# Kernel tuning notes

Hardware: AMD Instinct MI355X
Metric: run time of the kernel (lower is better)

The kernel has to match this reference:

```python
import jax, jax.numpy as jnp
import numpy as np

SUB = 40   # subframe_size
NSUB = 4   # nb_subframes


def _glu(x, w):
    return x * jax.nn.sigmoid(x @ w.T)


def _gru(x, h, w_ih, w_hh):
    # torch.nn.GRUCell (bias=False): gates ordered r, z, n
    H = h.shape[-1]
    gi = x @ w_ih.T
    gh = h @ w_hh.T
    r = jax.nn.sigmoid(gi[:, :H] + gh[:, :H])
    z = jax.nn.sigmoid(gi[:, H:2 * H] + gh[:, H:2 * H])
    n = jnp.tanh(gi[:, 2 * H:] + r * gh[:, 2 * H:])
    return (1.0 - z) * n + z * h


def _fargan_forward(features, period, p):
    B, T, _ = features.shape
    period = jnp.clip(period, 32, 254)

    # ---- FARGANCond ----
    f = features[:, 2:, :]                               # [B, T-2, 20]
    pidx = jnp.clip(period[:, 2:] - 32, 0, 223)
    pe = p['pembed'][pidx]                               # [B, T-2, 12]
    x = jnp.tanh(jnp.concatenate([f, pe], -1) @ p['fd1_w'].T)   # [B, T-2, 64]
    y = jax.lax.conv_general_dilated(
        x.transpose(0, 2, 1), p['fconv1_w'], (1,), 'VALID',
        dimension_numbers=('NCH', 'OIH', 'NCH'))
    y = jnp.tanh(y).transpose(0, 2, 1)                   # [B, T-4, 128]
    cond = jnp.tanh(y @ p['fd2_w'].T)                    # [B, T-4, 320]

    nb_frames = T - 4
    cond_steps = cond.reshape(B, nb_frames, NSUB, 80)
    cond_steps = cond_steps.transpose(1, 2, 0, 3).reshape(nb_frames * NSUB, B, 80)
    pitch = period[:, 3:3 + nb_frames]                   # conv-center aligned pitch
    pitch_steps = jnp.repeat(pitch.T, NSUB, axis=0)      # [steps, B]

    rng = jnp.arange(SUB + 4)

    def step(carry, inp):
        exc_mem, prev_pred, s1, s2, s3, fwc_state = carry
        cond80, per = inp
        gain = 0.2 + 0.8 * jax.nn.sigmoid(cond80 @ p['cg_w'].T + p['cg_b'])
        gain = jnp.clip(gain, 0.001, 20.0)               # [B, 1]
        idx = 256 - per[:, None] + rng[None, :] - 2
        idx = idx - (idx >= 256) * per[:, None]
        idx = jnp.clip(idx, 0, 255)
        pred = jnp.take_along_axis(exc_mem, idx, axis=1) / (1e-5 + gain)  # [B, 44]
        prev = exc_mem[:, -SUB:] / (1e-5 + gain)         # [B, 40]
        tmp = jnp.concatenate([cond80, pred, prev], 1)   # [B, 164]
        fpitch = pred[:, 2:-2]                           # [B, 40]
        xcat = jnp.concatenate([fwc_state, tmp], 1)      # [B, 328]
        fwc_out = _glu(jnp.tanh(xcat @ p['fwc_w'].T), p['fwc_glu_w'])  # [B, 192]
        new_fwc_state = xcat[:, 164:]
        pg = jax.nn.sigmoid(fwc_out @ p['gout_w'].T + p['gout_b'])     # [B, 4]
        s1n = _gru(jnp.concatenate([fwc_out, pg[:, 0:1] * fpitch, prev], 1), s1, p['g1_ih'], p['g1_hh'])
        g1 = _glu(s1n, p['glu1_w'])
        s2n = _gru(jnp.concatenate([g1, pg[:, 1:2] * fpitch, prev], 1), s2, p['g2_ih'], p['g2_hh'])
        g2 = _glu(s2n, p['glu2_w'])
        s3n = _gru(jnp.concatenate([g2, pg[:, 2:3] * fpitch, prev], 1), s3, p['g3_ih'], p['g3_hh'])
        g3 = _glu(s3n, p['glu3_w'])
        skip_in = jnp.concatenate([g1, g2, g3, fwc_out, pg[:, 3:4] * fpitch, prev], 1)  # [B, 688+80]
        skip = _glu(jnp.tanh(skip_in @ p['skip_w'].T), p['skip_glu_w'])
        sig = jnp.tanh(skip @ p['sig_w'].T) * gain       # [B, 40]
        exc_mem = jnp.concatenate([exc_mem[:, SUB:], sig], 1)
        prev_pred = jnp.concatenate([prev_pred[:, SUB:], fpitch], 1)
        return (exc_mem, prev_pred, s1n, s2n, s3n, new_fwc_state), sig

    dt = features.dtype
    carry0 = (jnp.zeros((B, 256), dt), jnp.zeros((B, 256), dt),
              jnp.zeros((B, 160), dt), jnp.zeros((B, 128), dt),
              jnp.zeros((B, 128), dt), jnp.zeros((B, 164), dt))
    _, sigs = jax.lax.scan(jax.checkpoint(step), carry0, (cond_steps, pitch_steps))
    return sigs.transpose(1, 0, 2).reshape(B, -1)        # [B, nb_frames*160]


def _w(key, out_dim, in_dim):
    return jax.random.normal(key, (out_dim, in_dim), jnp.float32) / np.sqrt(in_dim)


def setup_inputs() -> dict:
    key = jax.random.key(0)
    ks = jax.random.split(key, 24)
    B, T = 128, 504
    d = {}
    d['features'] = jax.random.normal(ks[0], (B, T, 20), jnp.float32)
    d['period'] = jax.random.randint(ks[1], (B, T), 32, 255)
    d['pembed'] = jax.random.normal(ks[2], (224, 12), jnp.float32) * 0.3
    d['fd1_w'] = _w(ks[3], 64, 32)
    d['fconv1_w'] = jax.random.normal(ks[4], (128, 64, 3), jnp.float32) / np.sqrt(192.0)
    d['fd2_w'] = _w(ks[5], 320, 128)
    d['cg_w'] = _w(ks[6], 1, 80)
    d['cg_b'] = jnp.zeros((1,), jnp.float32)
    d['fwc_w'] = _w(ks[7], 192, 328)
    d['fwc_glu_w'] = _w(ks[8], 192, 192)
    d['g1_ih'] = _w(ks[9], 480, 272)
    d['g1_hh'] = _w(ks[10], 480, 160)
    d['glu1_w'] = _w(ks[11], 160, 160)
    d['g2_ih'] = _w(ks[12], 384, 240)
    d['g2_hh'] = _w(ks[13], 384, 128)
    d['glu2_w'] = _w(ks[14], 128, 128)
    d['g3_ih'] = _w(ks[15], 384, 208)
    d['g3_hh'] = _w(ks[16], 384, 128)
    d['glu3_w'] = _w(ks[17], 128, 128)
    d['skip_w'] = _w(ks[18], 128, 688)
    d['skip_glu_w'] = _w(ks[19], 128, 128)
    d['sig_w'] = _w(ks[20], 40, 128)
    d['gout_w'] = _w(ks[21], 4, 192)
    d['gout_b'] = jnp.zeros((4,), jnp.float32)
    return d


def reference(features, period, pembed, fd1_w, fconv1_w, fd2_w, cg_w, cg_b,
              fwc_w, fwc_glu_w, g1_ih, g1_hh, glu1_w, g2_ih, g2_hh, glu2_w,
              g3_ih, g3_hh, glu3_w, skip_w, skip_glu_w, sig_w, gout_w, gout_b):
    p = dict(pembed=pembed, fd1_w=fd1_w, fconv1_w=fconv1_w, fd2_w=fd2_w,
             cg_w=cg_w, cg_b=cg_b, fwc_w=fwc_w, fwc_glu_w=fwc_glu_w,
             g1_ih=g1_ih, g1_hh=g1_hh, glu1_w=glu1_w,
             g2_ih=g2_ih, g2_hh=g2_hh, glu2_w=glu2_w,
             g3_ih=g3_ih, g3_hh=g3_hh, glu3_w=glu3_w,
             skip_w=skip_w, skip_glu_w=skip_glu_w, sig_w=sig_w,
             gout_w=gout_w, gout_b=gout_b)
    return _fargan_forward(features, period, p)
```

## Files before the change

### kernel.cpp

```cpp
#include <hip/hip_runtime.h>
#include <hip/hip_fp16.h>
#include <math.h>


#define DEV __device__ __forceinline__

DEV float sigm(float x) { return 1.0f / (1.0f + __expf(-x)); }
DEV float tanh_f(float x) { return 1.0f - 2.0f / (__expf(2.0f * x) + 1.0f); }

typedef _Float16 h2v __attribute__((ext_vector_type(2)));

#if defined(__has_builtin)
#if __has_builtin(__builtin_amdgcn_fdot2)
#define HAVE_FDOT2 1
#endif
#endif

DEV float fdot2(h2v a, h2v b, float c) {
#ifdef HAVE_FDOT2
    return __builtin_amdgcn_fdot2(a, b, c, false);
#else
    return c + (float)a[0] * (float)b[0] + (float)a[1] * (float)b[1];
#endif
}

constexpr size_t STEPS = 2000;
constexpr size_t OFF_X     = 0;
constexpr size_t OFF_Y     = 4200000;
constexpr size_t OFF_GAIN  = 12392000;
constexpr size_t OFF_CONDH = 12648000;
constexpr size_t OFF_W     = 22888000;

constexpr size_t W_FWC     = 0;
constexpr size_t W_FWCGLU  = W_FWC    + 192*352;
constexpr size_t W_GOUT    = W_FWCGLU + 192*192;
constexpr size_t W_G1IH    = W_GOUT   + 4*192;
constexpr size_t W_G1HH    = W_G1IH   + 480*272;
constexpr size_t W_GLU1    = W_G1HH   + 480*160;
constexpr size_t W_G2IH    = W_GLU1   + 160*160;
constexpr size_t W_G2HH    = W_G2IH   + 384*240;
constexpr size_t W_GLU2    = W_G2HH   + 384*128;
constexpr size_t W_G3IH    = W_GLU2   + 128*128;
constexpr size_t W_G3HH    = W_G3IH   + 384*208;
constexpr size_t W_GLU3    = W_G3HH   + 384*128;
constexpr size_t W_SKIP    = W_GLU3   + 128*128;
constexpr size_t W_SKIPGLU = W_SKIP   + 128*704;
constexpr size_t W_SIG     = W_SKIPGLU+ 128*128;

constexpr int WL_FWCGLU = 0;
constexpr int WL_GLU2   = 4608;
constexpr int WL_GLU3   = 6656;
constexpr int WL_TOT    = 8704;

__global__ void k_pack_h(const float* __restrict__ src, __half* __restrict__ dst,
                         int OUT, int K, int KP8) {
    int t = blockIdx.x * 256 + threadIdx.x;
    if (t >= OUT * KP8) return;
    int j = t % OUT;
    int k8 = t / OUT;
    __half* d = dst + (size_t)t * 8;
#pragma unroll
    for (int i = 0; i < 8; ++i) {
        int k = k8 * 8 + i;
        d[i] = (k < K) ? __float2half(src[(size_t)j * K + k]) : __float2half(0.0f);
    }
}

__global__ void k_feat(const float* __restrict__ features, const int* __restrict__ period,
                       const float* __restrict__ pembed, const float* __restrict__ fd1,
                       float* __restrict__ xbuf) {
    int t = blockIdx.x * 256 + threadIdx.x;
    const int total = 128 * 502 * 64;
    if (t >= total) return;
    int o = t & 63;
    int r = t >> 6;
    int ft = r % 502;
    int b = r / 502;
    const float* f = features + ((size_t)b * 504 + ft + 2) * 20;
    int per = period[b * 504 + ft + 2];
    per = min(max(per, 32), 254);
    const float* pe = pembed + (per - 32) * 12;
    const float* w = fd1 + o * 32;
    float acc = 0.0f;
#pragma unroll
    for (int i = 0; i < 20; ++i) acc += f[i] * w[i];
#pragma unroll
    for (int i = 0; i < 12; ++i) acc += pe[i] * w[20 + i];
    xbuf[t] = tanh_f(acc);
}

__global__ void k_conv(const float* __restrict__ xbuf, const float* __restrict__ fconv1,
                       float* __restrict__ ybuf) {
    int t = blockIdx.x * 256 + threadIdx.x;
    const int total = 128 * 500 * 128;
    if (t >= total) return;
    int oc = t & 127;
    int r = t >> 7;
    int tt = r % 500;
    int b = r / 500;
    const float* xp = xbuf + ((size_t)b * 502 + tt) * 64;
    const float* w = fconv1 + oc * 192;
    float acc = 0.0f;
#pragma unroll 8
    for (int i = 0; i < 64; ++i) {
        acc += xp[i] * w[i * 3 + 0];
        acc += xp[64 + i] * w[i * 3 + 1];
        acc += xp[128 + i] * w[i * 3 + 2];
    }
    ybuf[t] = tanh_f(acc);
}

__global__ void k_cond(const float* __restrict__ ybuf, const float* __restrict__ fd2,
                       __half* __restrict__ cond) {
    int b = blockIdx.x / 50;
    int t0 = (blockIdx.x % 50) * 10;
    int tid = threadIdx.x;
    __shared__ float yl[1280];
    for (int i = tid; i < 1280; i += 320)
        yl[i] = ybuf[((size_t)b * 500 + t0) * 128 + i];
    __syncthreads();
    const float* w = fd2 + tid * 128;
    float acc[10];
#pragma unroll
    for (int q = 0; q < 10; ++q) acc[q] = 0.0f;
#pragma unroll 4
    for (int k = 0; k < 128; ++k) {
        float wv = w[k];
#pragma unroll
        for (int q = 0; q < 10; ++q) acc[q] += wv * yl[q * 128 + k];
    }
#pragma unroll
    for (int q = 0; q < 10; ++q)
        cond[((size_t)b * 500 + t0 + q) * 320 + tid] = __float2half(tanh_f(acc[q]));
}

__global__ void k_gain(const __half* __restrict__ cond, const float* __restrict__ cgw,
                       const float* __restrict__ cgb, float* __restrict__ gains) {
    int t = blockIdx.x * 256 + threadIdx.x;
    const int total = 128 * 2000;
    if (t >= total) return;
    int s = t % 2000;
    int b = t / 2000;
    int frame = s >> 2, sub = s & 3;
    const __half* c = cond + ((size_t)b * 500 + frame) * 320 + sub * 80;
    float acc = 0.0f;
#pragma unroll 8
    for (int i = 0; i < 80; ++i) acc += __half2float(c[i]) * cgw[i];
    float g = 0.2f + 0.8f * sigm(acc + cgb[0]);
    g = fminf(20.0f, fmaxf(0.001f, g));
    gains[t] = g;
}

DEV void dot8h(uint4 w, uint4 x, float& a0, float& a1) {
    const h2v* wv = (const h2v*)&w;
    const h2v* xv = (const h2v*)&x;
    a0 = fdot2(wv[0], xv[0], a0);
    a1 = fdot2(wv[1], xv[1], a1);
    a0 = fdot2(wv[2], xv[2], a0);
    a1 = fdot2(wv[3], xv[3], a1);
}

template <int OUT, int KP8, int S>
DEV void mv_partial(const uint4* __restrict__ WT, const __half* __restrict__ x,
                    float* __restrict__ part, int tid) {
    static_assert(KP8 % S == 0, "KP8 % S");
    static_assert(OUT * S <= 1024, "threads");
    constexpr int KS8 = KP8 / S;
    if (tid < OUT * S) {
        int j = tid % OUT;
        int sl = tid / OUT;
        const uint4* w = WT + (size_t)sl * KS8 * OUT + j;
        const uint4* xx = (const uint4*)x + (size_t)sl * KS8;
        float a0 = 0.0f, a1 = 0.0f;
#pragma unroll 4
        for (int k = 0; k < KS8; ++k) dot8h(w[(size_t)k * OUT], xx[k], a0, a1);
        part[tid] = a0 + a1;
    }
}

template <int OUT, int KP8, int S>
DEV void mv_partial_l(const uint4* wl, const __half* __restrict__ x,
                      float* __restrict__ part, int tid) {
    constexpr int KS8 = KP8 / S;
    if (tid < OUT * S) {
        int j = tid % OUT;
        int sl = tid / OUT;
        const uint4* w = wl + (size_t)sl * KS8 * OUT + j;
        const uint4* xx = (const uint4*)x + (size_t)sl * KS8;
        float a0 = 0.0f, a1 = 0.0f;
#pragma unroll
        for (int k = 0; k < KS8; ++k) dot8h(w[(size_t)k * OUT], xx[k], a0, a1);
        part[tid] = a0 + a1;
    }
}

template <int OUT, int KP8A, int KP8B>
DEV void gru_partial(const uint4* __restrict__ wa, const __half* __restrict__ xa,
                     const uint4* __restrict__ wb, const __half* __restrict__ xb,
                     float* __restrict__ pa, float* __restrict__ pb, int tid) {
    static_assert((KP8A % 2 == 0) && (KP8B % 2 == 0), "even");
    constexpr int KA = KP8A / 2, KB = KP8B / 2;
    if (tid < OUT * 2) {
        int j = tid % OUT;
        int sl = tid / OUT;
        {
            const uint4* w = wa + (size_t)sl * KA * OUT + j;
            const uint4* xx = (const uint4*)xa + (size_t)sl * KA;
            float a0 = 0.0f, a1 = 0.0f;
#pragma unroll 4
            for (int k = 0; k < KA; ++k) dot8h(w[(size_t)k * OUT], xx[k], a0, a1);
            pa[tid] = a0 + a1;
        }
        {
            const uint4* w = wb + (size_t)sl * KB * OUT + j;
            const uint4* xx = (const uint4*)xb + (size_t)sl * KB;
            float b0 = 0.0f, b1 = 0.0f;
#pragma unroll 4
            for (int k = 0; k < KB; ++k) dot8h(w[(size_t)k * OUT], xx[k], b0, b1);
            pb[tid] = b0 + b1;
        }
    }
}

template <int H>
DEV void gru_update(const float* __restrict__ pa, const float* __restrict__ pb,
                    float* __restrict__ s, __half* __restrict__ sh, int tid) {
    constexpr int OUT = 3 * H;
    if (tid < H) {
        float gi_r = pa[tid] + pa[OUT + tid];
        float gh_r = pb[tid] + pb[OUT + tid];
        float gi_z = pa[H + tid] + pa[OUT + H + tid];
        float gh_z = pb[H + tid] + pb[OUT + H + tid];
        float gi_n = pa[2 * H + tid] + pa[OUT + 2 * H + tid];
        float gh_n = pb[2 * H + tid] + pb[OUT + 2 * H + tid];
        float r = sigm(gi_r + gh_r);
        float z = sigm(gi_z + gh_z);
        float n = tanh_f(gi_n + r * gh_n);
        float v = (1.0f - z) * n + z * s[tid];
        s[tid] = v;
        sh[tid] = __float2half(v);
    }
}

__global__ __launch_bounds__(1024) void fargan_main(const float* __restrict__ ws,
                                                    const int* __restrict__ period,
                                                    const float* __restrict__ goutb,
                                                    float* __restrict__ out) {
    const int b = blockIdx.x;
    const int tid = threadIdx.x;

    const __half* cond = (const __half*)(ws + OFF_CONDH);
    const float* gains = ws + OFF_GAIN;
    const __half* whb  = (const __half*)(ws + OFF_W);
    const uint4* wFWC     = (const uint4*)(whb + W_FWC);
    const uint4* wFWCGLU  = (const uint4*)(whb + W_FWCGLU);
    const uint4* wGOUT    = (const uint4*)(whb + W_GOUT);
    const uint4* wG1IH    = (const uint4*)(whb + W_G1IH);
    const uint4* wG1HH    = (const uint4*)(whb + W_G1HH);
    const uint4* wGLU1    = (const uint4*)(whb + W_GLU1);
    const uint4* wG2IH    = (const uint4*)(whb + W_G2IH);
    const uint4* wG2HH    = (const uint4*)(whb + W_G2HH);
    const uint4* wGLU2    = (const uint4*)(whb + W_GLU2);
    const uint4* wG3IH    = (const uint4*)(whb + W_G3IH);
    const uint4* wG3HH    = (const uint4*)(whb + W_G3HH);
    const uint4* wGLU3    = (const uint4*)(whb + W_GLU3);
    const uint4* wSKIP    = (const uint4*)(whb + W_SKIP);
    const uint4* wSKIPGLU = (const uint4*)(whb + W_SKIPGLU);
    const uint4* wSIG     = (const uint4*)(whb + W_SIG);

    __shared__ __align__(16) uint4 wlds[WL_TOT];

    __shared__ __align__(16) __half xcat_h[352];
    __shared__ __align__(16) __half inb_h[272];
    __shared__ __align__(16) __half fwcpre_h[192], fwcout_h[192];
    __shared__ __align__(16) __half s1_h[160], s2_h[128], s3_h[128];
    __shared__ __align__(16) __half g1_h[160], g2_h[128], g3_h[128];
    __shared__ __align__(16) __half skipin_h[704], skippre_h[128], skipout_h[128];
    __shared__ __align__(16) float exc[256];
    __shared__ __align__(16) float s1[160], s2[128], s3[128];
    __shared__ __align__(16) float partA[1024], partB[1024];
    __shared__ __align__(16) float fwcpre[192];
    __shared__ __align__(16) float pg[4];
    __shared__ __align__(16) float skippre[128];
    __shared__ __align__(16) float sigraw[40];

    for (int i = tid; i < 4608; i += 1024) wlds[WL_FWCGLU + i] = wFWCGLU[i];
    for (int i = tid; i < 2048; i += 1024) wlds[WL_GLU2 + i] = wGLU2[i];
    for (int i = tid; i < 2048; i += 1024) wlds[WL_GLU3 + i] = wGLU3[i];

    const int j2 = tid % 384;
    const int sl2 = (tid < 768) ? (tid / 384) : 0;
    const uint4* g2b = wG2HH + (size_t)sl2 * 8 * 384 + j2;
    const uint4 c0 = g2b[0 * 384];
    const uint4 c1 = g2b[1 * 384];
    const uint4 c2 = g2b[2 * 384];
    const uint4 c3 = g2b[3 * 384];
    const uint4 c4 = g2b[4 * 384];
    const uint4 c5 = g2b[5 * 384];
    const uint4 c6 = g2b[6 * 384];
    const uint4 c7 = g2b[7 * 384];

    for (int i = tid; i < 256; i += 1024) exc[i] = 0.0f;
    if (tid < 160) { s1[tid] = 0.0f; s1_h[tid] = __float2half(0.0f); }
    if (tid < 128) { s2[tid] = 0.0f; s3[tid] = 0.0f;
                     s2_h[tid] = __float2half(0.0f); s3_h[tid] = __float2half(0.0f); }
    if (tid < 164) xcat_h[tid] = __float2half(0.0f);
    if (tid >= 328 && tid < 352) xcat_h[tid] = __float2half(0.0f);
    if (tid >= 688 && tid < 704) skipin_h[tid] = __float2half(0.0f);
    __syncthreads();

    for (int s = 0; s < (int)STEPS; ++s) {
        const int frame = s >> 2;
        const float gain = gains[(size_t)b * 2000 + s];
        const float ig = 1.0f / (1e-5f + gain);
        int per = period[b * 504 + 3 + frame];
        per = min(max(per, 32), 254);

        if (tid < 80) {
            xcat_h[164 + tid] = cond[((size_t)b * 500 + frame) * 320 + (s & 3) * 80 + tid];
        } else if (tid >= 128 && tid < 172) {
            int j = tid - 128;
            int idx = 254 - per + j;
            if (idx >= 256) idx -= per;
            idx = min(255, max(0, idx));
            xcat_h[244 + j] = __float2half(exc[idx] * ig);
        } else if (tid >= 192 && tid < 232) {
            xcat_h[288 + tid - 192] = __float2half(exc[216 + tid - 192] * ig);
        }
        __syncthreads();

        mv_partial<192, 44, 4>(wFWC, xcat_h, partA, tid);
        __syncthreads();
        if (tid < 192) {
            float a = partA[tid] + partA[192 + tid] + partA[384 + tid] + partA[576 + tid];
            float t = tanh_f(a);
            fwcpre[tid] = t;
            fwcpre_h[tid] = __float2half(t);
        }
        __syncthreads();

        mv_partial_l<192, 24, 4>(wlds + WL_FWCGLU, fwcpre_h, partA, tid);
        if (tid >= 768 && tid < 800) {
            int t2 = tid - 768;
            int j = t2 & 3, sl = t2 >> 2;
            const uint4* w = wGOUT + (sl * 3) * 4 + j;
            const uint4* xx = (const uint4*)fwcpre_h + sl * 3;
            float a0 = 0.0f, a1 = 0.0f;
#pragma unroll
            for (int k = 0; k < 3; ++k) dot8h(w[k * 4], xx[k], a0, a1);
            partB[t2] = a0 + a1;
        } else if (tid >= 832 && tid < 996) {
            xcat_h[tid - 832] = xcat_h[tid - 832 + 164];
        }
        __syncthreads();

        if (tid < 192) {
            float a = partA[tid] + partA[192 + tid] + partA[384 + tid] + partA[576 + tid];
            float v = fwcpre[tid] * sigm(a);
            __half vh = __float2half(v);
            fwcout_h[tid] = vh;
            inb_h[tid] = vh;
        } else if (tid < 232) {
            float a = goutb[0];
#pragma unroll
            for (int sl = 0; sl < 8; ++sl) a += partB[sl * 4];
            inb_h[tid] = __float2half(sigm(a) * __half2float(xcat_h[246 + tid - 192]));
        } else if (tid < 272) {
            inb_h[tid] = xcat_h[288 + tid - 232];
        } else if (tid >= 960 && tid < 964) {
            int j = tid - 960;
            float a = goutb[j];
#pragma unroll
            for (int sl = 0; sl < 8; ++sl) a += partB[sl * 4 + j];
            pg[j] = sigm(a);
        }
        __syncthreads();

        gru_partial<480, 34, 20>(wG1IH, inb_h, wG1HH, s1_h, partA, partB, tid);
        __syncthreads();
        gru_update<160>(partA, partB, s1, s1_h, tid);
        __syncthreads();

        mv_partial<160, 20, 4>(wGLU1, s1_h, partA, tid);
        __syncthreads();
        if (tid < 160) {
            float a = partA[tid] + partA[160 + tid] + partA[320 + tid] + partA[480 + tid];
            float v = s1[tid] * sigm(a);
            __half vh = __float2half(v);
            g1_h[tid] = vh;
            inb_h[tid] = vh;
        } else if (tid < 200) {
            inb_h[tid] = __float2half(pg[1] * __half2float(xcat_h[246 + tid - 160]));
        } else if (tid < 240) {
            inb_h[tid] = xcat_h[288 + tid - 200];
        }
        __syncthreads();

        if (tid < 768) {
            constexpr int KA = 15;
            {
                const uint4* w = wG2IH + (size_t)sl2 * KA * 384 + j2;
                const uint4* xx = (const uint4*)inb_h + (size_t)sl2 * KA;
                float a0 = 0.0f, a1 = 0.0f;
#pragma unroll 4
                for (int k = 0; k < KA; ++k) dot8h(w[(size_t)k * 384], xx[k], a0, a1);
                partA[tid] = a0 + a1;
            }
            {
                const uint4* xb = (const uint4*)s2_h + (size_t)sl2 * 8;
                float b0 = 0.0f, b1 = 0.0f;
                dot8h(c0, xb[0], b0, b1);
                dot8h(c1, xb[1], b0, b1);
                dot8h(c2, xb[2], b0, b1);
                dot8h(c3, xb[3], b0, b1);
                dot8h(c4, xb[4], b0, b1);
                dot8h(c5, xb[5], b0, b1);
                dot8h(c6, xb[6], b0, b1);
                dot8h(c7, xb[7], b0, b1);
                partB[tid] = b0 + b1;
            }
        }
        __syncthreads();
        gru_update<128>(partA, partB, s2, s2_h, tid);
        __syncthreads();

        mv_partial_l<128, 16, 8>(wlds + WL_GLU2, s2_h, partA, tid);
        __syncthreads();
        if (tid < 128) {
            float a = 0.0f;
#pragma unroll
            for (int sl = 0; sl < 8; ++sl) a += partA[sl * 128 + tid];
            float v = s2[tid] * sigm(a);
            __half vh = __float2half(v);
            g2_h[tid] = vh;
            inb_h[tid] = vh;
        } else if (tid < 168) {
            inb_h[tid] = __float2half(pg[2] * __half2float(xcat_h[246 + tid - 128]));
        } else if (tid < 208) {
            inb_h[tid] = xcat_h[288 + tid - 168];
        }
        __syncthreads();

        gru_partial<384, 26, 16>(wG3IH, inb_h, wG3HH, s3_h, partA, partB, tid);
        __syncthreads();
        gru_update<128>(partA, partB, s3, s3_h, tid);
        __syncthreads();

        mv_partial_l<128, 16, 8>(wlds + WL_GLU3, s3_h, partA, tid);
        __syncthreads();
        if (tid < 128) {
            float a = 0.0f;
#pragma unroll
            for (int sl = 0; sl < 8; ++sl) a += partA[sl * 128 + tid];
            float v = s3[tid] * sigm(a);
            __half vh = __float2half(v);
            g3_h[tid] = vh;
            skipin_h[288 + tid] = vh;
        } else if (tid < 288) {
            skipin_h[tid - 128] = g1_h[tid - 128];
        } else if (tid < 416) {
            skipin_h[160 + tid - 288] = g2_h[tid - 288];
        } else if (tid < 608) {
            skipin_h[tid] = fwcout_h[tid - 416];
        } else if (tid < 648) {
            skipin_h[tid] = __float2half(pg[3] * __half2float(xcat_h[246 + tid - 608]));
        } else if (tid < 688) {
            skipin_h[tid] = xcat_h[288 + tid - 648];
        }
        __syncthreads();

        mv_partial<128, 88, 8>(wSKIP, skipin_h, partA, tid);
        __syncthreads();
        if (tid < 128) {
            float a = 0.0f;
#pragma unroll
            for (int sl = 0; sl < 8; ++sl) a += partA[sl * 128 + tid];
            float t = tanh_f(a);
            skippre[tid] = t;
            skippre_h[tid] = __float2half(t);
        }
        __syncthreads();

        mv_partial<128, 16, 8>(wSKIPGLU, skippre_h, partA, tid);
        __syncthreads();
        if (tid < 128) {
            float a = 0.0f;
#pragma unroll
            for (int sl = 0; sl < 8; ++sl) a += partA[sl * 128 + tid];
            skipout_h[tid] = __float2half(skippre[tid] * sigm(a));
        }
        __syncthreads();

        mv_partial<40, 16, 8>(wSIG, skipout_h, partA, tid);
        __syncthreads();
        float keep = (tid < 216) ? exc[tid + 40] : 0.0f;
        if (tid < 40) {
            float a = 0.0f;
#pragma unroll
            for (int sl = 0; sl < 8; ++sl) a += partA[sl * 40 + tid];
            sigraw[tid] = tanh_f(a) * gain;
        }
        __syncthreads();
        if (tid < 216) {
            exc[tid] = keep;
        } else if (tid < 256) {
            float sv = sigraw[tid - 216];
            exc[tid] = sv;
            out[(size_t)b * 80000 + (size_t)s * 40 + (tid - 216)] = sv;
        }
        __syncthreads();
    }
}

extern "C" void kernel_launch(void* const* d_in, const int* in_sizes, int n_in,
                              void* d_out, int out_size, void* d_ws, size_t ws_size,
                              hipStream_t stream) {
    const float* features = (const float*)d_in[0];
    const int*   period   = (const int*)d_in[1];
    const float* pembed   = (const float*)d_in[2];
    const float* fd1_w    = (const float*)d_in[3];
    const float* fconv1_w = (const float*)d_in[4];
    const float* fd2_w    = (const float*)d_in[5];
    const float* cg_w     = (const float*)d_in[6];
    const float* cg_b     = (const float*)d_in[7];
    const float* fwc_w    = (const float*)d_in[8];
    const float* fwc_glu  = (const float*)d_in[9];
    const float* g1_ih    = (const float*)d_in[10];
    const float* g1_hh    = (const float*)d_in[11];
    const float* glu1_w   = (const float*)d_in[12];
    const float* g2_ih    = (const float*)d_in[13];
    const float* g2_hh    = (const float*)d_in[14];
    const float* glu2_w   = (const float*)d_in[15];
    const float* g3_ih    = (const float*)d_in[16];
    const float* g3_hh    = (const float*)d_in[17];
    const float* glu3_w   = (const float*)d_in[18];
    const float* skip_w   = (const float*)d_in[19];
    const float* skip_glu = (const float*)d_in[20];
    const float* sig_w    = (const float*)d_in[21];
    const float* gout_w   = (const float*)d_in[22];
    const float* gout_b   = (const float*)d_in[23];

    float* ws = (float*)d_ws;
    float* out = (float*)d_out;
    __half* wh = (__half*)(ws + OFF_W);

    struct PW { const float* src; size_t off; int out, k, kpad; };
    const PW pws[15] = {
        {fwc_w,    W_FWC,     192, 328, 352}, {fwc_glu, W_FWCGLU, 192, 192, 192},
        {gout_w,   W_GOUT,      4, 192, 192}, {g1_ih,   W_G1IH,   480, 272, 272},
        {g1_hh,    W_G1HH,    480, 160, 160}, {glu1_w,  W_GLU1,   160, 160, 160},
        {g2_ih,    W_G2IH,    384, 240, 240}, {g2_hh,   W_G2HH,   384, 128, 128},
        {glu2_w,   W_GLU2,    128, 128, 128}, {g3_ih,   W_G3IH,   384, 208, 208},
        {g3_hh,    W_G3HH,    384, 128, 128}, {glu3_w,  W_GLU3,   128, 128, 128},
        {skip_w,   W_SKIP,    128, 688, 704}, {skip_glu,W_SKIPGLU,128, 128, 128},
        {sig_w,    W_SIG,      40, 128, 128},
    };
    for (int i = 0; i < 15; ++i) {
        int kp8 = pws[i].kpad / 8;
        int n = pws[i].out * kp8;
        k_pack_h<<<(n + 255) / 256, 256, 0, stream>>>(pws[i].src, wh + pws[i].off,
                                                      pws[i].out, pws[i].k, kp8);
    }

    {
        int n = 128 * 502 * 64;
        k_feat<<<(n + 255) / 256, 256, 0, stream>>>(features, period, pembed, fd1_w,
                                                    ws + OFF_X);
    }
    {
        int n = 128 * 500 * 128;
        k_conv<<<(n + 255) / 256, 256, 0, stream>>>(ws + OFF_X, fconv1_w, ws + OFF_Y);
    }
    k_cond<<<128 * 50, 320, 0, stream>>>(ws + OFF_Y, fd2_w, (__half*)(ws + OFF_CONDH));
    {
        int n = 128 * 2000;
        k_gain<<<(n + 255) / 256, 256, 0, stream>>>((const __half*)(ws + OFF_CONDH),
                                                    cg_w, cg_b, ws + OFF_GAIN);
    }

    fargan_main<<<128, 1024, 0, stream>>>(ws, period, gout_b, out);
}
```

Before: 34.19 ms.

## Interleave K-split weight layout and reduce partial sums with wave shuffles

Weights are repacked so the K-slices of one output row sit in adjacent lanes. Each matvec then reduces its partial sums with __shfl_xor instead of writing them to shared memory and summing in a separate phase. This removes many __syncthreads barriers and shared-memory round trips per subframe step in the sequential recurrent loop. It also fuses the post-processing (tanh, sigmoid gating, the gain output) into the matvec phase and changes some split factors, for example GLU2 and GLU3 go from 8 slices to 4, which may lower parallelism per matvec.

```diff
diff --git a/kernel.cpp b/kernel.cpp
--- a/kernel.cpp
+++ b/kernel.cpp
@@ -53,15 +53,19 @@
 constexpr int WL_TOT    = 8704;
 
 __global__ void k_pack_h(const float* __restrict__ src, __half* __restrict__ dst,
-                         int OUT, int K, int KP8) {
+                         int OUT, int K, int KP8, int S) {
     int t = blockIdx.x * 256 + threadIdx.x;
     if (t >= OUT * KP8) return;
     int j = t % OUT;
-    int k8 = t / OUT;
-    __half* d = dst + (size_t)t * 8;
+    int c = t / OUT;
+    int KS8 = KP8 / S;
+    int sl = c / KS8;
+    int kk = c % KS8;
+    size_t di = (size_t)kk * (OUT * S) + (size_t)j * S + sl;
+    __half* d = dst + di * 8;
 #pragma unroll
     for (int i = 0; i < 8; ++i) {
-        int k = k8 * 8 + i;
+        int k = c * 8 + i;
         d[i] = (k < K) ? __float2half(src[(size_t)j * K + k]) : __float2half(0.0f);
     }
 }
@@ -161,81 +165,74 @@
 }
 
 template <int OUT, int KP8, int S>
-DEV void mv_partial(const uint4* __restrict__ WT, const __half* __restrict__ x,
-                    float* __restrict__ part, int tid) {
-    static_assert(KP8 % S == 0, "KP8 % S");
-    static_assert(OUT * S <= 1024, "threads");
+DEV float mv_w(const uint4* __restrict__ WT, const __half* __restrict__ x, int tid) {
+    static_assert(64 % S == 0, "S divides wave");
     constexpr int KS8 = KP8 / S;
-    if (tid < OUT * S) {
-        int j = tid % OUT;
-        int sl = tid / OUT;
-        const uint4* w = WT + (size_t)sl * KS8 * OUT + j;
-        const uint4* xx = (const uint4*)x + (size_t)sl * KS8;
+    constexpr int TH = OUT * S;
+    const uint4* w = WT + tid;
+    const uint4* xx = (const uint4*)x + (tid % S) * KS8;
+    float a0 = 0.0f, a1 = 0.0f;
+#pragma unroll 4
+    for (int k = 0; k < KS8; ++k) dot8h(w[(size_t)k * TH], xx[k], a0, a1);
+    float p = a0 + a1;
+    if (S >= 2) p += __shfl_xor(p, 1);
+    if (S >= 4) p += __shfl_xor(p, 2);
+    if (S >= 8) p += __shfl_xor(p, 4);
+    return p;
+}
+
+template <int OUT, int KP8, int S>
+DEV float mv_w_l(const uint4* wl, const __half* __restrict__ x, int tid) {
+    constexpr int KS8 = KP8 / S;
+    constexpr int TH = OUT * S;
+    const uint4* w = wl + tid;
+    const uint4* xx = (const uint4*)x + (tid % S) * KS8;
+    float a0 = 0.0f, a1 = 0.0f;
+#pragma unroll
+    for (int k = 0; k < KS8; ++k) dot8h(w[(size_t)k * TH], xx[k], a0, a1);
+    float p = a0 + a1;
+    if (S >= 2) p += __shfl_xor(p, 1);
+    if (S >= 4) p += __shfl_xor(p, 2);
+    if (S >= 8) p += __shfl_xor(p, 4);
+    return p;
+}
+
+template <int OUT, int KP8A, int KP8B>
+DEV void gru_w(const uint4* __restrict__ wa, const __half* __restrict__ xa,
+               const uint4* __restrict__ wb, const __half* __restrict__ xb,
+               float* __restrict__ gi, float* __restrict__ gh, int tid) {
+    constexpr int KA = KP8A / 2, KB = KP8B / 2;
+    constexpr int TH = OUT * 2;
+    const int sl = tid & 1, j = tid >> 1;
+    float pA, pB;
+    {
+        const uint4* w = wa + tid;
+        const uint4* xx = (const uint4*)xa + sl * KA;
         float a0 = 0.0f, a1 = 0.0f;
 #pragma unroll 4
-        for (int k = 0; k < KS8; ++k) dot8h(w[(size_t)k * OUT], xx[k], a0, a1);
-        part[tid] = a0 + a1;
-    }
-}
-
-template <int OUT, int KP8, int S>
-DEV void mv_partial_l(const uint4* wl, const __half* __restrict__ x,
-                      float* __restrict__ part, int tid) {
-    constexpr int KS8 = KP8 / S;
-    if (tid < OUT * S) {
-        int j = tid % OUT;
-        int sl = tid / OUT;
-        const uint4* w = wl + (size_t)sl * KS8 * OUT + j;
-        const uint4* xx = (const uint4*)x + (size_t)sl * KS8;
-        float a0 = 0.0f, a1 = 0.0f;
-#pragma unroll
-        for (int k = 0; k < KS8; ++k) dot8h(w[(size_t)k * OUT], xx[k], a0, a1);
-        part[tid] = a0 + a1;
-    }
-}
-
-template <int OUT, int KP8A, int KP8B>
-DEV void gru_partial(const uint4* __restrict__ wa, const __half* __restrict__ xa,
-                     const uint4* __restrict__ wb, const __half* __restrict__ xb,
-                     float* __restrict__ pa, float* __restrict__ pb, int tid) {
-    static_assert((KP8A % 2 == 0) && (KP8B % 2 == 0), "even");
-    constexpr int KA = KP8A / 2, KB = KP8B / 2;
-    if (tid < OUT * 2) {
-        int j = tid % OUT;
-        int sl = tid / OUT;
-        {
-            const uint4* w = wa + (size_t)sl * KA * OUT + j;
-            const uint4* xx = (const uint4*)xa + (size_t)sl * KA;
-            float a0 = 0.0f, a1 = 0.0f;
+        for (int k = 0; k < KA; ++k) dot8h(w[(size_t)k * TH], xx[k], a0, a1);
+        pA = a0 + a1;
+        pA += __shfl_xor(pA, 1);
+    }
+    {
+        const uint4* w = wb + tid;
+        const uint4* xx = (const uint4*)xb + sl * KB;
+        float b0 = 0.0f, b1 = 0.0f;
 #pragma unroll 4
-            for (int k = 0; k < KA; ++k) dot8h(w[(size_t)k * OUT], xx[k], a0, a1);
-            pa[tid] = a0 + a1;
-        }
-        {
-            const uint4* w = wb + (size_t)sl * KB * OUT + j;
-            const uint4* xx = (const uint4*)xb + (size_t)sl * KB;
-            float b0 = 0.0f, b1 = 0.0f;
-#pragma unroll 4
-            for (int k = 0; k < KB; ++k) dot8h(w[(size_t)k * OUT], xx[k], b0, b1);
-            pb[tid] = b0 + b1;
-        }
-    }
+        for (int k = 0; k < KB; ++k) dot8h(w[(size_t)k * TH], xx[k], b0, b1);
+        pB = b0 + b1;
+        pB += __shfl_xor(pB, 1);
+    }
+    if (sl == 0) { gi[j] = pA; gh[j] = pB; }
 }
 
 template <int H>
-DEV void gru_update(const float* __restrict__ pa, const float* __restrict__ pb,
-                    float* __restrict__ s, __half* __restrict__ sh, int tid) {
-    constexpr int OUT = 3 * H;
+DEV void gru_upd(const float* __restrict__ gi, const float* __restrict__ gh,
+                 float* __restrict__ s, __half* __restrict__ sh, int tid) {
     if (tid < H) {
-        float gi_r = pa[tid] + pa[OUT + tid];
-        float gh_r = pb[tid] + pb[OUT + tid];
-        float gi_z = pa[H + tid] + pa[OUT + H + tid];
-        float gh_z = pb[H + tid] + pb[OUT + H + tid];
-        float gi_n = pa[2 * H + tid] + pa[OUT + 2 * H + tid];
-        float gh_n = pb[2 * H + tid] + pb[OUT + 2 * H + tid];
-        float r = sigm(gi_r + gh_r);
-        float z = sigm(gi_z + gh_z);
-        float n = tanh_f(gi_n + r * gh_n);
+        float r = sigm(gi[tid] + gh[tid]);
+        float z = sigm(gi[H + tid] + gh[H + tid]);
+        float n = tanh_f(gi[2 * H + tid] + r * gh[2 * H + tid]);
         float v = (1.0f - z) * n + z * s[tid];
         s[tid] = v;
         sh[tid] = __float2half(v);
@@ -278,27 +275,25 @@
     __shared__ __align__(16) __half skipin_h[704], skippre_h[128], skipout_h[128];
     __shared__ __align__(16) float exc[256];
     __shared__ __align__(16) float s1[160], s2[128], s3[128];
-    __shared__ __align__(16) float partA[1024], partB[1024];
+    __shared__ __align__(16) float gi_f[480], gh_f[480];
     __shared__ __align__(16) float fwcpre[192];
     __shared__ __align__(16) float pg[4];
     __shared__ __align__(16) float skippre[128];
-    __shared__ __align__(16) float sigraw[40];
 
     for (int i = tid; i < 4608; i += 1024) wlds[WL_FWCGLU + i] = wFWCGLU[i];
     for (int i = tid; i < 2048; i += 1024) wlds[WL_GLU2 + i] = wGLU2[i];
     for (int i = tid; i < 2048; i += 1024) wlds[WL_GLU3 + i] = wGLU3[i];
 
-    const int j2 = tid % 384;
-    const int sl2 = (tid < 768) ? (tid / 384) : 0;
-    const uint4* g2b = wG2HH + (size_t)sl2 * 8 * 384 + j2;
-    const uint4 c0 = g2b[0 * 384];
-    const uint4 c1 = g2b[1 * 384];
-    const uint4 c2 = g2b[2 * 384];
-    const uint4 c3 = g2b[3 * 384];
-    const uint4 c4 = g2b[4 * 384];
-    const uint4 c5 = g2b[5 * 384];
-    const uint4 c6 = g2b[6 * 384];
-    const uint4 c7 = g2b[7 * 384];
+    const int tcl = (tid < 768) ? tid : 0;
+    const uint4* g2b = wG2HH + tcl;
+    const uint4 c0 = g2b[0 * 768];
+    const uint4 c1 = g2b[1 * 768];
+    const uint4 c2 = g2b[2 * 768];
+    const uint4 c3 = g2b[3 * 768];
+    const uint4 c4 = g2b[4 * 768];
+    const uint4 c5 = g2b[5 * 768];
+    const uint4 c6 = g2b[6 * 768];
+    const uint4 c7 = g2b[7 * 768];
 
     for (int i = tid; i < 256; i += 1024) exc[i] = 0.0f;
     if (tid < 160) { s1[tid] = 0.0f; s1_h[tid] = __float2half(0.0f); }
@@ -316,6 +311,7 @@
         int per = period[b * 504 + 3 + frame];
         per = min(max(per, 32), 254);
 
+        float keep = (tid < 216) ? exc[tid + 40] : 0.0f;
         if (tid < 80) {
             xcat_h[164 + tid] = cond[((size_t)b * 500 + frame) * 320 + (s & 3) * 80 + tid];
         } else if (tid >= 128 && tid < 172) {
@@ -329,185 +325,180 @@
         }
         __syncthreads();
 
-        mv_partial<192, 44, 4>(wFWC, xcat_h, partA, tid);
-        __syncthreads();
-        if (tid < 192) {
-            float a = partA[tid] + partA[192 + tid] + partA[384 + tid] + partA[576 + tid];
-            float t = tanh_f(a);
-            fwcpre[tid] = t;
-            fwcpre_h[tid] = __float2half(t);
-        }
-        __syncthreads();
-
-        mv_partial_l<192, 24, 4>(wlds + WL_FWCGLU, fwcpre_h, partA, tid);
-        if (tid >= 768 && tid < 800) {
+        if (tid < 768) {
+            float p = mv_w<192, 44, 4>(wFWC, xcat_h, tid);
+            if ((tid & 3) == 0) {
+                int j = tid >> 2;
+                float t = tanh_f(p);
+                fwcpre[j] = t;
+                fwcpre_h[j] = __float2half(t);
+            }
+        }
+        __syncthreads();
+
+        if (tid < 768) {
+            float p = mv_w_l<192, 24, 4>(wlds + WL_FWCGLU, fwcpre_h, tid);
+            if ((tid & 3) == 0) {
+                int j = tid >> 2;
+                float v = fwcpre[j] * sigm(p);
+                __half vh = __float2half(v);
+                fwcout_h[j] = vh;
+                inb_h[j] = vh;
+            }
+        } else if (tid < 800) {
             int t2 = tid - 768;
-            int j = t2 & 3, sl = t2 >> 2;
-            const uint4* w = wGOUT + (sl * 3) * 4 + j;
-            const uint4* xx = (const uint4*)fwcpre_h + sl * 3;
+            const uint4* w = wGOUT + t2;
+            const uint4* xx = (const uint4*)fwcpre_h + (t2 & 7) * 3;
             float a0 = 0.0f, a1 = 0.0f;
-#pragma unroll
-            for (int k = 0; k < 3; ++k) dot8h(w[k * 4], xx[k], a0, a1);
-            partB[t2] = a0 + a1;
+            dot8h(w[0 * 32], xx[0], a0, a1);
+            dot8h(w[1 * 32], xx[1], a0, a1);
+            dot8h(w[2 * 32], xx[2], a0, a1);
+            float p = a0 + a1;
+            p += __shfl_xor(p, 1);
+            p += __shfl_xor(p, 2);
+            p += __shfl_xor(p, 4);
+            if ((t2 & 7) == 0) pg[t2 >> 3] = sigm(p + goutb[t2 >> 3]);
         } else if (tid >= 832 && tid < 996) {
             xcat_h[tid - 832] = xcat_h[tid - 832 + 164];
         }
         __syncthreads();
 
-        if (tid < 192) {
-            float a = partA[tid] + partA[192 + tid] + partA[384 + tid] + partA[576 + tid];
-            float v = fwcpre[tid] * sigm(a);
-            __half vh = __float2half(v);
-            fwcout_h[tid] = vh;
-            inb_h[tid] = vh;
-        } else if (tid < 232) {
-            float a = goutb[0];
-#pragma unroll
-            for (int sl = 0; sl < 8; ++sl) a += partB[sl * 4];
-            inb_h[tid] = __float2half(sigm(a) * __half2float(xcat_h[246 + tid - 192]));
-        } else if (tid < 272) {
-            inb_h[tid] = xcat_h[288 + tid - 232];
-        } else if (tid >= 960 && tid < 964) {
-            int j = tid - 960;
-            float a = goutb[j];
-#pragma unroll
-            for (int sl = 0; sl < 8; ++sl) a += partB[sl * 4 + j];
-            pg[j] = sigm(a);
-        }
-        __syncthreads();
-
-        gru_partial<480, 34, 20>(wG1IH, inb_h, wG1HH, s1_h, partA, partB, tid);
-        __syncthreads();
-        gru_update<160>(partA, partB, s1, s1_h, tid);
-        __syncthreads();
-
-        mv_partial<160, 20, 4>(wGLU1, s1_h, partA, tid);
-        __syncthreads();
-        if (tid < 160) {
-            float a = partA[tid] + partA[160 + tid] + partA[320 + tid] + partA[480 + tid];
-            float v = s1[tid] * sigm(a);
-            __half vh = __float2half(v);
-            g1_h[tid] = vh;
-            inb_h[tid] = vh;
-        } else if (tid < 200) {
-            inb_h[tid] = __float2half(pg[1] * __half2float(xcat_h[246 + tid - 160]));
-        } else if (tid < 240) {
-            inb_h[tid] = xcat_h[288 + tid - 200];
+        if (tid < 80) {
+            inb_h[192 + tid] = (tid < 40)
+                ? __float2half(pg[0] * __half2float(xcat_h[246 + tid]))
+                : xcat_h[288 + tid - 40];
+        }
+        __syncthreads();
+
+        if (tid < 960)
+            gru_w<480, 34, 20>(wG1IH, inb_h, wG1HH, s1_h, gi_f, gh_f, tid);
+        __syncthreads();
+        gru_upd<160>(gi_f, gh_f, s1, s1_h, tid);
+        __syncthreads();
+
+        if (tid < 640) {
+            float p = mv_w<160, 20, 4>(wGLU1, s1_h, tid);
+            if ((tid & 3) == 0) {
+                int j = tid >> 2;
+                float v = s1[j] * sigm(p);
+                __half vh = __float2half(v);
+                g1_h[j] = vh;
+                inb_h[j] = vh;
+            }
+        } else if (tid < 720) {
+            int t = tid - 640;
+            inb_h[160 + t] = (t < 40)
+                ? __float2half(pg[1] * __half2float(xcat_h[246 + t]))
+                : xcat_h[288 + t - 40];
         }
         __syncthreads();
 
         if (tid < 768) {
-            constexpr int KA = 15;
+            const int sl = tid & 1, j = tid >> 1;
+            float pA, pB;
             {
-                const uint4* w = wG2IH + (size_t)sl2 * KA * 384 + j2;
-                const uint4* xx = (const uint4*)inb_h + (size_t)sl2 * KA;
+                const uint4* w = wG2IH + tid;
+                const uint4* xx = (const uint4*)inb_h + sl * 15;
                 float a0 = 0.0f, a1 = 0.0f;
 #pragma unroll 4
-                for (int k = 0; k < KA; ++k) dot8h(w[(size_t)k * 384], xx[k], a0, a1);
-                partA[tid] = a0 + a1;
+                for (int k = 0; k < 15; ++k) dot8h(w[(size_t)k * 768], xx[k], a0, a1);
+                pA = a0 + a1;
+                pA += __shfl_xor(pA, 1);
             }
             {
-                const uint4* xb = (const uint4*)s2_h + (size_t)sl2 * 8;
+                const uint4* xx = (const uint4*)s2_h + sl * 8;
                 float b0 = 0.0f, b1 = 0.0f;
-                dot8h(c0, xb[0], b0, b1);
-                dot8h(c1, xb[1], b0, b1);
-                dot8h(c2, xb[2], b0, b1);
-                dot8h(c3, xb[3], b0, b1);
-                dot8h(c4, xb[4], b0, b1);
-                dot8h(c5, xb[5], b0, b1);
-                dot8h(c6, xb[6], b0, b1);
-                dot8h(c7, xb[7], b0, b1);
-                partB[tid] = b0 + b1;
-            }
-        }
-        __syncthreads();
-        gru_update<128>(partA, partB, s2, s2_h, tid);
-        __syncthreads();
-
-        mv_partial_l<128, 16, 8>(wlds + WL_GLU2, s2_h, partA, tid);
-        __syncthreads();
-        if (tid < 128) {
-            float a = 0.0f;
-#pragma unroll
-            for (int sl = 0; sl < 8; ++sl) a += partA[sl * 128 + tid];
-            float v = s2[tid] * sigm(a);
-            __half vh = __float2half(v);
-            g2_h[tid] = vh;
-            inb_h[tid] = vh;
-        } else if (tid < 168) {
-            inb_h[tid] = __float2half(pg[2] * __half2float(xcat_h[246 + tid - 128]));
-        } else if (tid < 208) {
-            inb_h[tid] = xcat_h[288 + tid - 168];
-        }
-        __syncthreads();
-
-        gru_partial<384, 26, 16>(wG3IH, inb_h, wG3HH, s3_h, partA, partB, tid);
-        __syncthreads();
-        gru_update<128>(partA, partB, s3, s3_h, tid);
-        __syncthreads();
-
-        mv_partial_l<128, 16, 8>(wlds + WL_GLU3, s3_h, partA, tid);
-        __syncthreads();
-        if (tid < 128) {
-            float a = 0.0f;
-#pragma unroll
-            for (int sl = 0; sl < 8; ++sl) a += partA[sl * 128 + tid];
-            float v = s3[tid] * sigm(a);
-            __half vh = __float2half(v);
-            g3_h[tid] = vh;
-            skipin_h[288 + tid] = vh;
-        } else if (tid < 288) {
-            skipin_h[tid - 128] = g1_h[tid - 128];
-        } else if (tid < 416) {
-            skipin_h[160 + tid - 288] = g2_h[tid - 288];
-        } else if (tid < 608) {
-            skipin_h[tid] = fwcout_h[tid - 416];
-        } else if (tid < 648) {
-            skipin_h[tid] = __float2half(pg[3] * __half2float(xcat_h[246 + tid - 608]));
-        } else if (tid < 688) {
-            skipin_h[tid] = xcat_h[288 + tid - 648];
-        }
-        __syncthreads();
-
-        mv_partial<128, 88, 8>(wSKIP, skipin_h, partA, tid);
-        __syncthreads();
-        if (tid < 128) {
-            float a = 0.0f;
-#pragma unroll
-            for (int sl = 0; sl < 8; ++sl) a += partA[sl * 128 + tid];
-            float t = tanh_f(a);
-            skippre[tid] = t;
-            skippre_h[tid] = __float2half(t);
-        }
-        __syncthreads();
-
-        mv_partial<128, 16, 8>(wSKIPGLU, skippre_h, partA, tid);
-        __syncthreads();
-        if (tid < 128) {
-            float a = 0.0f;
-#pragma unroll
-            for (int sl = 0; sl < 8; ++sl) a += partA[sl * 128 + tid];
-            skipout_h[tid] = __float2half(skippre[tid] * sigm(a));
-        }
-        __syncthreads();
-
-        mv_partial<40, 16, 8>(wSIG, skipout_h, partA, tid);
-        __syncthreads();
-        float keep = (tid < 216) ? exc[tid + 40] : 0.0f;
-        if (tid < 40) {
-            float a = 0.0f;
-#pragma unroll
-            for (int sl = 0; sl < 8; ++sl) a += partA[sl * 40 + tid];
-            sigraw[tid] = tanh_f(a) * gain;
-        }
-        __syncthreads();
-        if (tid < 216) {
-            exc[tid] = keep;
-        } else if (tid < 256) {
-            float sv = sigraw[tid - 216];
-            exc[tid] = sv;
-            out[(size_t)b * 80000 + (size_t)s * 40 + (tid - 216)] = sv;
-        }
+                dot8h(c0, xx[0], b0, b1);
+                dot8h(c1, xx[1], b0, b1);
+                dot8h(c2, xx[2], b0, b1);
+                dot8h(c3, xx[3], b0, b1);
+                dot8h(c4, xx[4], b0, b1);
+                dot8h(c5, xx[5], b0, b1);
+                dot8h(c6, xx[6], b0, b1);
+                dot8h(c7, xx[7], b0, b1);
+                pB = b0 + b1;
+                pB += __shfl_xor(pB, 1);
+            }
+            if (sl == 0) { gi_f[j] = pA; gh_f[j] = pB; }
+        }
+        __syncthreads();
+        gru_upd<128>(gi_f, gh_f, s2, s2_h, tid);
+        __syncthreads();
+
+        if (tid < 512) {
+            float p = mv_w_l<128, 16, 4>(wlds + WL_GLU2, s2_h, tid);
+            if ((tid & 3) == 0) {
+                int j = tid >> 2;
+                float v = s2[j] * sigm(p);
+                __half vh = __float2half(v);
+                g2_h[j] = vh;
+                inb_h[j] = vh;
+            }
+        } else if (tid < 592) {
+            int t = tid - 512;
+            inb_h[128 + t] = (t < 40)
+                ? __float2half(pg[2] * __half2float(xcat_h[246 + t]))
+                : xcat_h[288 + t - 40];
+        }
+        __syncthreads();
+
+        if (tid < 768)
+            gru_w<384, 26, 16>(wG3IH, inb_h, wG3HH, s3_h, gi_f, gh_f, tid);
+        __syncthreads();
+        gru_upd<128>(gi_f, gh_f, s3, s3_h, tid);
+        __syncthreads();
+
+        if (tid < 512) {
+            float p = mv_w_l<128, 16, 4>(wlds + WL_GLU3, s3_h, tid);
+            if ((tid & 3) == 0) {
+                int j = tid >> 2;
+                float v = s3[j] * sigm(p);
+                __half vh = __float2half(v);
+                g3_h[j] = vh;
+                skipin_h[288 + j] = vh;
+            }
+        } else {
+            for (int i = tid - 512; i < 560; i += 512) {
+                if (i < 160)       skipin_h[i] = g1_h[i];
+                else if (i < 288)  skipin_h[i] = g2_h[i - 160];
+                else if (i < 480)  skipin_h[416 + (i - 288)] = fwcout_h[i - 288];
+                else if (i < 520)  skipin_h[608 + (i - 480)] =
+                    __float2half(pg[3] * __half2float(xcat_h[246 + (i - 480)]));
+                else               skipin_h[648 + (i - 520)] = xcat_h[288 + (i - 520)];
+            }
+        }
+        __syncthreads();
+
+        {
+            float p = mv_w<128, 88, 8>(wSKIP, skipin_h, tid);
+            if ((tid & 7) == 0) {
+                int j = tid >> 3;
+                float t = tanh_f(p);
+                skippre[j] = t;
+                skippre_h[j] = __float2half(t);
+            }
+        }
+        __syncthreads();
+
+        {
+            float p = mv_w<128, 16, 8>(wSKIPGLU, skippre_h, tid);
+            if ((tid & 7) == 0) {
+                int j = tid >> 3;
+                skipout_h[j] = __float2half(skippre[j] * sigm(p));
+            }
+        }
+        __syncthreads();
+
+        if (tid < 320) {
+            float p = mv_w<40, 16, 8>(wSIG, skipout_h, tid);
+            if ((tid & 7) == 0) {
+                int j = tid >> 3;
+                float sv = tanh_f(p) * gain;
+                exc[216 + j] = sv;
+                out[(size_t)b * 80000 + (size_t)s * 40 + j] = sv;
+            }
+        }
+        if (tid < 216) exc[tid] = keep;
         __syncthreads();
     }
 }
@@ -544,22 +535,23 @@
     float* out = (float*)d_out;
     __half* wh = (__half*)(ws + OFF_W);
 
-    struct PW { const float* src; size_t off; int out, k, kpad; };
+    struct PW { const float* src; size_t off; int out, k, kpad, S; };
     const PW pws[15] = {
-        {fwc_w,    W_FWC,     192, 328, 352}, {fwc_glu, W_FWCGLU, 192, 192, 192},
-        {gout_w,   W_GOUT,      4, 192, 192}, {g1_ih,   W_G1IH,   480, 272, 272},
-        {g1_hh,    W_G1HH,    480, 160, 160}, {glu1_w,  W_GLU1,   160, 160, 160},
-        {g2_ih,    W_G2IH,    384, 240, 240}, {g2_hh,   W_G2HH,   384, 128, 128},
-        {glu2_w,   W_GLU2,    128, 128, 128}, {g3_ih,   W_G3IH,   384, 208, 208},
-        {g3_hh,    W_G3HH,    384, 128, 128}, {glu3_w,  W_GLU3,   128, 128, 128},
-        {skip_w,   W_SKIP,    128, 688, 704}, {skip_glu,W_SKIPGLU,128, 128, 128},
-        {sig_w,    W_SIG,      40, 128, 128},
+        {fwc_w,    W_FWC,     192, 328, 352, 4}, {fwc_glu, W_FWCGLU, 192, 192, 192, 4},
+        {gout_w,   W_GOUT,      4, 192, 192, 8}, {g1_ih,   W_G1IH,   480, 272, 272, 2},
+        {g1_hh,    W_G1HH,    480, 160, 160, 2}, {glu1_w,  W_GLU1,   160, 160, 160, 4},
+        {g2_ih,    W_G2IH,    384, 240, 240, 2}, {g2_hh,   W_G2HH,   384, 128, 128, 2},
+        {glu2_w,   W_GLU2,    128, 128, 128, 4}, {g3_ih,   W_G3IH,   384, 208, 208, 2},
+        {g3_hh,    W_G3HH,    384, 128, 128, 2}, {glu3_w,  W_GLU3,   128, 128, 128, 4},
+        {skip_w,   W_SKIP,    128, 688, 704, 8}, {skip_glu,W_SKIPGLU,128, 128, 128, 8},
+        {sig_w,    W_SIG,      40, 128, 128, 8},
     };
     for (int i = 0; i < 15; ++i) {
         int kp8 = pws[i].kpad / 8;
         int n = pws[i].out * kp8;
         k_pack_h<<<(n + 255) / 256, 256, 0, stream>>>(pws[i].src, wh + pws[i].off,
-                                                      pws[i].out, pws[i].k, kp8);
+                                                      pws[i].out, pws[i].k, kp8,
+                                                      pws[i].S);
     }
 
     {
```

After: 34.12 ms. Within noise of the previous version (-0.2%).
